# Kernel tuning notes

Hardware: AMD Instinct MI355X
Metric: run time of the kernel (lower is better)

The kernel has to match this reference:

```python
import jax, jax.numpy as jnp
import numpy as np

ADAPT_RATE = 0.05


def setup_inputs() -> dict:
    key = jax.random.key(0)
    k1, k2, k3 = jax.random.split(key, 3)
    B, T, DIN, DOUT = 64, 256, 1024, 1024
    x = jax.random.normal(k1, (B, T, DIN), dtype=jnp.float32)
    W = jax.random.normal(k2, (DOUT, DIN), dtype=jnp.float32) / np.sqrt(DIN)
    b = jax.random.normal(k3, (DOUT,), dtype=jnp.float32) * 0.01
    threshold = jnp.ones((DOUT,), dtype=jnp.float32)
    return {"x": x, "W": W, "b": b, "threshold": threshold}


def reference(x, W, b, threshold):
    # Precompute the per-timestep linear once as a single big GEMM: [B,T,O]
    pre = jnp.einsum('bti,oi->bto', x, W) + b
    B, T, O = pre.shape

    def step(carry, pre_t):
        mem, thr = carry
        mem = mem + pre_t                       # membrane accumulate [B,O]
        s = (mem >= thr).astype(pre_t.dtype)    # hard threshold spike
        # adaptive threshold: in-place .data update in torch (no grad path)
        thr = thr + ADAPT_RATE * (s.mean(axis=0) - 0.5)
        mem = mem * (1.0 - s)                   # reset where spiked
        return (mem, thr), s

    mem0 = jnp.zeros((B, O), dtype=x.dtype)
    (_, _), spikes = jax.lax.scan(step, (mem0, threshold), jnp.swapaxes(pre, 0, 1))
    return jnp.swapaxes(spikes, 0, 1)  # [B,T,O]
```

## Files before the change

### kernel.cpp

```cpp
#include <hip/hip_runtime.h>

#define B_ 64
#define T_ 256
#define DIN_ 1024
#define DOUT_ 1024

typedef int v4i  __attribute__((ext_vector_type(4)));
typedef int v16i __attribute__((ext_vector_type(16)));

#define PRE_BYTES 134217728ULL
#define XS_BYTES  83886080ULL
#define WSL_BYTES 5242880ULL
#define SPM_BYTES 2097152ULL

__device__ __forceinline__ void async_copy16(const void* g, void* l) {
    __builtin_amdgcn_global_load_lds(
        (const __attribute__((address_space(1))) void*)g,
        (__attribute__((address_space(3))) void*)l, 16, 0, 0);
}

__global__ __launch_bounds__(256) void snn_split_x(
    const float* __restrict__ x, char* __restrict__ xs)
{
    const int W    = blockIdx.x * 4 + (threadIdx.x >> 6);
    const int lane = threadIdx.x & 63;
    const int mt = W & 1, kt = (W >> 1) & 31, t0 = W >> 6;
    const int m = lane & 31, kh = lane >> 5;
    const int b = mt * 32 + m;

    const float* src = x + ((size_t)b * T_ + t0) * DIN_ + kt * 32 + kh * 16;
    float f[16];
    *(float4*)(f)      = *(const float4*)(src);
    *(float4*)(f + 4)  = *(const float4*)(src + 4);
    *(float4*)(f + 8)  = *(const float4*)(src + 8);
    *(float4*)(f + 12) = *(const float4*)(src + 12);

    unsigned pk[4][4];
#pragma unroll
    for (int s = 0; s < 4; ++s)
        pk[s][0] = pk[s][1] = pk[s][2] = pk[s][3] = 0u;
#pragma unroll
    for (int j = 0; j < 16; ++j) {
        float v = f[j] * 0.125f;
#pragma unroll
        for (int s = 0; s < 4; ++s) {
            const float ml = (s == 0) ? 64.f : 128.f;
            const float sv = __builtin_rintf(v * ml);
            v = v * ml - sv;
            const int iv = (int)sv;
            pk[s][j >> 2] |= ((unsigned)iv & 0xffu) << ((j & 3) * 8);
        }
    }
#pragma unroll
    for (int s = 0; s < 4; ++s) {
        char* dst = xs + (size_t)(((s * 256 + t0) * 32 + kt) * 2 + mt) * 1024
                       + lane * 16;
        *(uint4*)dst = make_uint4(pk[s][0], pk[s][1], pk[s][2], pk[s][3]);
    }
}

__global__ __launch_bounds__(256) void snn_split_w(
    const float* __restrict__ Wt, char* __restrict__ wsl)
{
    const int W    = blockIdx.x * 4 + (threadIdx.x >> 6);
    const int lane = threadIdx.x & 63;
    const int kt = W & 31, ot = W >> 5;
    const int n = lane & 31, kh = lane >> 5;
    const int o = ot * 32 + n;

    const float* src = Wt + (size_t)o * DIN_ + kt * 32 + kh * 16;
    float f[16];
    *(float4*)(f)      = *(const float4*)(src);
    *(float4*)(f + 4)  = *(const float4*)(src + 4);
    *(float4*)(f + 8)  = *(const float4*)(src + 8);
    *(float4*)(f + 12) = *(const float4*)(src + 12);

    unsigned pk[4][4];
#pragma unroll
    for (int s = 0; s < 4; ++s)
        pk[s][0] = pk[s][1] = pk[s][2] = pk[s][3] = 0u;
#pragma unroll
    for (int j = 0; j < 16; ++j) {
        float v = f[j] * 4.0f;
#pragma unroll
        for (int s = 0; s < 4; ++s) {
            const float ml = (s == 0) ? 64.f : 128.f;
            const float sv = __builtin_rintf(v * ml);
            v = v * ml - sv;
            const int iv = (int)sv;
            pk[s][j >> 2] |= ((unsigned)iv & 0xffu) << ((j & 3) * 8);
        }
    }
#pragma unroll
    for (int s = 0; s < 4; ++s) {
        char* dst = wsl + (size_t)((s * 32 + ot) * 32 + kt) * 1024 + lane * 16;
        *(uint4*)dst = make_uint4(pk[s][0], pk[s][1], pk[s][2], pk[s][3]);
    }
}

__global__ __launch_bounds__(256, 4) void snn_gemm_i8(
    const char* __restrict__ xs, const char* __restrict__ wsl,
    const float* __restrict__ bias, double* __restrict__ pre)
{
    __shared__ __align__(16) char ldsA[3][8 * 1024];
    __shared__ __align__(16) char ldsB[2][8 * 1024];
    const int t0 = blockIdx.x >> 4;
    const int oc = blockIdx.x & 15;
    const int tid = threadIdx.x;
    const int lane = tid & 63;
    const int ws = __builtin_amdgcn_readfirstlane(tid >> 6);
    const int wm = ws >> 1;
    const int wo = ws & 1;
    const int lo = lane * 16;

    v16i acc[4];
#pragma unroll
    for (int g = 0; g < 4; ++g)
#pragma unroll
        for (int r = 0; r < 16; ++r) acc[g][r] = 0;

    const char* sgA = xs  + (size_t)(t0 * 64 + ws) * 1024 + lo;
    const char* sgB = wsl + (size_t)((oc * 2 + (ws - 2)) * 32) * 1024 + lo;

    if (ws < 2) {
#pragma unroll
        for (int s = 0; s < 4; ++s)
            async_copy16(sgA + (size_t)s * 16777216, &ldsA[0][(ws * 4 + s) * 1024]);
#pragma unroll
        for (int s = 0; s < 4; ++s)
            async_copy16(sgA + (size_t)s * 16777216 + 2048,
                         &ldsA[1][(ws * 4 + s) * 1024]);
    } else {
#pragma unroll
        for (int s = 0; s < 4; ++s)
            async_copy16(sgB + (size_t)s * 1048576,
                         &ldsB[0][((ws - 2) * 4 + s) * 1024]);
    }

    int rdA = 0;
    int stA = 2;
    for (int kt = 0; kt < 32; ++kt) {
        if (ws < 2) {
            if (kt < 31) asm volatile("s_waitcnt vmcnt(4)" ::: "memory");
            else         asm volatile("s_waitcnt vmcnt(0)" ::: "memory");
        } else {
            asm volatile("s_waitcnt vmcnt(0)" ::: "memory");
        }
        __builtin_amdgcn_s_barrier();
        asm volatile("" ::: "memory");

        if (ws < 2) {
            if (kt + 2 < 32) {
                const size_t ko = (size_t)(kt + 2) * 2048;
#pragma unroll
                for (int s = 0; s < 4; ++s)
                    async_copy16(sgA + (size_t)s * 16777216 + ko,
                                 &ldsA[stA][(ws * 4 + s) * 1024]);
            }
        } else {
            if (kt + 1 < 32) {
                const size_t ko = (size_t)(kt + 1) * 1024;
#pragma unroll
                for (int s = 0; s < 4; ++s)
                    async_copy16(sgB + (size_t)s * 1048576 + ko,
                                 &ldsB[(kt + 1) & 1][((ws - 2) * 4 + s) * 1024]);
            }
        }

        const char* bufA = ldsA[rdA];
        const char* bufB = ldsB[kt & 1];
        v4i a[4], b[4];
#pragma unroll
        for (int s = 0; s < 4; ++s)
            a[s] = *(const v4i*)(bufA + (wm * 4 + s) * 1024 + lo);
#pragma unroll
        for (int s = 0; s < 4; ++s)
            b[s] = *(const v4i*)(bufB + (wo * 4 + s) * 1024 + lo);

        __builtin_amdgcn_s_setprio(1);
#define MF(I, J)                                                               \
        acc[(I) + (J)] = __builtin_amdgcn_mfma_i32_32x32x32_i8(                \
            a[I], b[J], acc[(I) + (J)], 0, 0, 0)
        MF(0, 3); MF(0, 2); MF(0, 1);
        MF(1, 2); MF(1, 1); MF(1, 0);
        MF(2, 1); MF(2, 0); MF(0, 0);
        MF(3, 0);
#undef MF
        __builtin_amdgcn_s_setprio(0);

        rdA = (rdA == 2) ? 0 : rdA + 1;
        stA = (stA == 2) ? 0 : stA + 1;
    }

    const int n = lane & 31, lh = lane >> 5;
    const int o = oc * 64 + wo * 32 + n;
    const double bv = (double)bias[o];
    double* dst = pre + ((size_t)t0 * DOUT_ + o) * 64 + wm * 32;
#pragma unroll
    for (int r = 0; r < 16; ++r) {
        const int row = (r & 3) + 8 * (r >> 2) + 4 * lh;
        double v = (double)acc[3][r];
        v = v * 0.0078125 + (double)acc[2][r];
        v = v * 0.0078125 + (double)acc[1][r];
        v = v * 0.0078125 + (double)acc[0][r];
        dst[row] = v * 0x1p-11 + bv;
    }
}

__global__ __launch_bounds__(256, 2) void snn_gemm_fb(
    const float* __restrict__ x, const float* __restrict__ W,
    const float* __restrict__ bias, double* __restrict__ pre)
{
    __shared__ float smem[2][8 * 72 + 8 * 256];
    const int t0 = blockIdx.x & 255;
    const int o0 = blockIdx.x >> 8;
    const int tid = threadIdx.x;
    const int to = tid & 31;
    const int tb = tid >> 5;

    double acc[8][8];
#pragma unroll
    for (int i = 0; i < 8; ++i)
#pragma unroll
        for (int j = 0; j < 8; ++j) acc[i][j] = 0.0;

    const int arow = tid >> 2;
    const int ak2  = (tid & 3) * 2;
    const float* xg = x + (size_t)(t0 + 256 * arow) * DIN_ + ak2;
    const float* wg = W + (size_t)(o0 * 256 + tid) * DIN_;

    float2 f2  = *(const float2*)(xg);
    float4 bq0 = *(const float4*)(wg);
    float4 bq1 = *(const float4*)(wg + 4);

    for (int kc = 0; kc < DIN_ / 8; ++kc) {
        float* base = smem[kc & 1];
        float (*AsF)[72]  = (float(*)[72])base;
        float (*BsF)[256] = (float(*)[256])(base + 8 * 72);
        AsF[ak2 + 0][arow] = f2.x;
        AsF[ak2 + 1][arow] = f2.y;
        BsF[0][tid] = bq0.x;  BsF[1][tid] = bq0.y;
        BsF[2][tid] = bq0.z;  BsF[3][tid] = bq0.w;
        BsF[4][tid] = bq1.x;  BsF[5][tid] = bq1.y;
        BsF[6][tid] = bq1.z;  BsF[7][tid] = bq1.w;
        __syncthreads();
        if (kc + 1 < DIN_ / 8) {
            f2  = *(const float2*)(xg + (kc + 1) * 8);
            bq0 = *(const float4*)(wg + (kc + 1) * 8);
            bq1 = *(const float4*)(wg + (kc + 1) * 8 + 4);
        }
#pragma unroll
        for (int k = 0; k < 8; ++k) {
            const float4 af0 = *(const float4*)&AsF[k][tb * 8];
            const float4 af1 = *(const float4*)&AsF[k][tb * 8 + 4];
            const float4 bf0 = *(const float4*)&BsF[k][to * 4];
            const float4 bf1 = *(const float4*)&BsF[k][128 + to * 4];
            double a[8], b[8];
            a[0] = (double)af0.x; a[1] = (double)af0.y;
            a[2] = (double)af0.z; a[3] = (double)af0.w;
            a[4] = (double)af1.x; a[5] = (double)af1.y;
            a[6] = (double)af1.z; a[7] = (double)af1.w;
            b[0] = (double)bf0.x; b[1] = (double)bf0.y;
            b[2] = (double)bf0.z; b[3] = (double)bf0.w;
            b[4] = (double)bf1.x; b[5] = (double)bf1.y;
            b[6] = (double)bf1.z; b[7] = (double)bf1.w;
#pragma unroll
            for (int i = 0; i < 8; ++i)
#pragma unroll
                for (int j = 0; j < 8; ++j)
                    acc[i][j] += a[i] * b[j];
        }
        __syncthreads();
    }

    double biasd[8];
#pragma unroll
    for (int j = 0; j < 8; ++j)
        biasd[j] = (double)bias[o0 * 256 + (j >> 2) * 128 + to * 4 + (j & 3)];
    double (*trans)[67] = (double(*)[67])smem[0];
    for (int c = 0; c < 16; ++c) {
        __syncthreads();
        const int j4  = c >> 3;
        const int tlo = (c & 7) * 4;
        if (to >= tlo && to < tlo + 4) {
#pragma unroll
            for (int p4 = 0; p4 < 4; ++p4) {
                const int r = (to - tlo) * 4 + p4;
                const int j = j4 * 4 + p4;
#pragma unroll
                for (int i = 0; i < 8; ++i)
                    trans[r][tb * 8 + i] = acc[i][j] + biasd[j];
            }
        }
        __syncthreads();
#pragma unroll
        for (int q = 0; q < 4; ++q) {
            const int idx = tid + 256 * q;
            const int b  = idx & 63;
            const int oc = idx >> 6;
            pre[(size_t)(t0 * DOUT_ + o0 * 256 + c * 16 + oc) * 64 + b] = trans[oc][b];
        }
    }
}

#define SCAN_LOAD(PV, TB)                                                      \
    do {                                                                       \
        _Pragma("unroll")                                                      \
        for (int j = 0; j < 16; ++j)                                           \
            PV[j] = p[(size_t)((TB) + j) * (DOUT_ * 64)];                      \
    } while (0)

#define SCAN_STEP(PV, TB)                                                      \
    do {                                                                       \
        _Pragma("unroll")                                                      \
        for (int j = 0; j < 16; ++j) {                                         \
            mem += PV[j];                                                      \
            const bool s = (mem >= thr);                                       \
            const unsigned long long msk = __ballot(s);                        \
            thr += 0.05 * ((double)__popcll(msk) * (1.0 / 64.0) - 0.5);        \
            if (spM) {                                                         \
                if (lane == 0) spM[(size_t)((TB) + j) * DOUT_ + o] = msk;      \
            } else {                                                           \
                outD[(size_t)lane * (T_ * DOUT_) +                             \
                     (size_t)((TB) + j) * DOUT_ + o] = s ? 1.0f : 0.0f;        \
            }                                                                  \
            mem = s ? 0.0 : mem;                                               \
        }                                                                      \
    } while (0)

__global__ __launch_bounds__(256) void snn_scan(
    const double* __restrict__ pre, const float* __restrict__ thr_in,
    unsigned long long* __restrict__ spM, float* __restrict__ outD)
{
    const int wid  = (blockIdx.x * blockDim.x + threadIdx.x) >> 6;
    const int lane = threadIdx.x & 63;
    if (wid >= DOUT_) return;
    const int o = wid;

    double mem = 0.0;
    double thr = (double)thr_in[o];
    const double* p = pre + (size_t)o * 64 + lane;

    double pvA[16], pvB[16];
    SCAN_LOAD(pvA, 0);
    for (int t = 0; t < T_; t += 32) {
        if (t + 16 < T_) SCAN_LOAD(pvB, t + 16);
        SCAN_STEP(pvA, t);
        if (t + 32 < T_) SCAN_LOAD(pvA, t + 32);
        SCAN_STEP(pvB, t + 16);
    }
}

__global__ __launch_bounds__(256) void snn_expand(
    const unsigned long long* __restrict__ spM, float* __restrict__ out)
{
    const int idx = blockIdx.x * 256 + threadIdx.x;
    const int og = idx & 255;
    const int t  = idx >> 8;
    const unsigned long long* mp = spM + (size_t)t * DOUT_ + og * 4;
    const unsigned long long m0 = mp[0], m1 = mp[1], m2 = mp[2], m3 = mp[3];
    float* op = out + (size_t)t * DOUT_ + og * 4;
#pragma unroll
    for (int b = 0; b < 64; ++b) {
        float4 v;
        v.x = (float)((m0 >> b) & 1ULL);
        v.y = (float)((m1 >> b) & 1ULL);
        v.z = (float)((m2 >> b) & 1ULL);
        v.w = (float)((m3 >> b) & 1ULL);
        *(float4*)(op + (size_t)b * (T_ * DOUT_)) = v;
    }
}

extern "C" void kernel_launch(void* const* d_in, const int* in_sizes, int n_in,
                              void* d_out, int out_size, void* d_ws, size_t ws_size,
                              hipStream_t stream) {
    const float* x    = (const float*)d_in[0];
    const float* W    = (const float*)d_in[1];
    const float* bias = (const float*)d_in[2];
    const float* thr  = (const float*)d_in[3];
    float* out = (float*)d_out;

    double* pre = (double*)d_ws;
    const size_t need = PRE_BYTES + XS_BYTES + WSL_BYTES + SPM_BYTES;

    if (ws_size >= need) {
        char* xs  = (char*)d_ws + PRE_BYTES;
        char* wsl = xs + XS_BYTES;
        unsigned long long* spM = (unsigned long long*)(wsl + WSL_BYTES);
        snn_split_x<<<4096, 256, 0, stream>>>(x, xs);
        snn_split_w<<<256, 256, 0, stream>>>(W, wsl);
        snn_gemm_i8<<<4096, 256, 0, stream>>>(xs, wsl, bias, pre);
        snn_scan<<<256, 256, 0, stream>>>(pre, thr, spM, nullptr);
        snn_expand<<<256, 256, 0, stream>>>(spM, out);
    } else {
        const bool two_stage = (ws_size >= PRE_BYTES + SPM_BYTES);
        unsigned long long* spM =
            two_stage ? (unsigned long long*)((char*)d_ws + PRE_BYTES) : nullptr;
        snn_gemm_fb<<<1024, 256, 0, stream>>>(x, W, bias, pre);
        snn_scan<<<256, 256, 0, stream>>>(pre, thr, spM, two_stage ? nullptr : out);
        if (two_stage)
            snn_expand<<<1024, 256, 0, stream>>>(spM, out);
    }
}
```

Before: 340.0 us.

## Replace LDS-staged async pipeline in int8 GEMM with direct register double-buffering

The int8 split-precision GEMM kernel no longer stages A and B tiles through LDS with global_load_lds, waitcnt and per-iteration barriers. Each wave now loads its own fragments straight from global memory into two register sets and alternates between them, overlapping the next tile's loads with the current MFMAs. This removes the barriers and LDS traffic but duplicates global loads across waves that share tiles (A is read by both wo waves, B by both wm waves) and raises register pressure, so launch bounds drop from 4 to 3 blocks per SIMD.

Result: slower. 372.7 us (+9.6%).

```diff
diff --git a/kernel.cpp b/kernel.cpp
--- a/kernel.cpp
+++ b/kernel.cpp
@@ -12,12 +12,6 @@
 #define XS_BYTES  83886080ULL
 #define WSL_BYTES 5242880ULL
 #define SPM_BYTES 2097152ULL
-
-__device__ __forceinline__ void async_copy16(const void* g, void* l) {
-    __builtin_amdgcn_global_load_lds(
-        (const __attribute__((address_space(1))) void*)g,
-        (__attribute__((address_space(3))) void*)l, 16, 0, 0);
-}
 
 __global__ __launch_bounds__(256) void snn_split_x(
     const float* __restrict__ x, char* __restrict__ xs)
@@ -98,12 +92,10 @@
     }
 }
 
-__global__ __launch_bounds__(256, 4) void snn_gemm_i8(
+__global__ __launch_bounds__(256, 3) void snn_gemm_i8(
     const char* __restrict__ xs, const char* __restrict__ wsl,
     const float* __restrict__ bias, double* __restrict__ pre)
 {
-    __shared__ __align__(16) char ldsA[3][8 * 1024];
-    __shared__ __align__(16) char ldsB[2][8 * 1024];
     const int t0 = blockIdx.x >> 4;
     const int oc = blockIdx.x & 15;
     const int tid = threadIdx.x;
@@ -119,78 +111,54 @@
 #pragma unroll
         for (int r = 0; r < 16; ++r) acc[g][r] = 0;
 
-    const char* sgA = xs  + (size_t)(t0 * 64 + ws) * 1024 + lo;
-    const char* sgB = wsl + (size_t)((oc * 2 + (ws - 2)) * 32) * 1024 + lo;
-
-    if (ws < 2) {
-#pragma unroll
-        for (int s = 0; s < 4; ++s)
-            async_copy16(sgA + (size_t)s * 16777216, &ldsA[0][(ws * 4 + s) * 1024]);
-#pragma unroll
-        for (int s = 0; s < 4; ++s)
-            async_copy16(sgA + (size_t)s * 16777216 + 2048,
-                         &ldsA[1][(ws * 4 + s) * 1024]);
-    } else {
-#pragma unroll
-        for (int s = 0; s < 4; ++s)
-            async_copy16(sgB + (size_t)s * 1048576,
-                         &ldsB[0][((ws - 2) * 4 + s) * 1024]);
-    }
-
-    int rdA = 0;
-    int stA = 2;
-    for (int kt = 0; kt < 32; ++kt) {
-        if (ws < 2) {
-            if (kt < 31) asm volatile("s_waitcnt vmcnt(4)" ::: "memory");
-            else         asm volatile("s_waitcnt vmcnt(0)" ::: "memory");
-        } else {
-            asm volatile("s_waitcnt vmcnt(0)" ::: "memory");
-        }
-        __builtin_amdgcn_s_barrier();
-        asm volatile("" ::: "memory");
-
-        if (ws < 2) {
-            if (kt + 2 < 32) {
-                const size_t ko = (size_t)(kt + 2) * 2048;
-#pragma unroll
-                for (int s = 0; s < 4; ++s)
-                    async_copy16(sgA + (size_t)s * 16777216 + ko,
-                                 &ldsA[stA][(ws * 4 + s) * 1024]);
-            }
-        } else {
-            if (kt + 1 < 32) {
-                const size_t ko = (size_t)(kt + 1) * 1024;
-#pragma unroll
-                for (int s = 0; s < 4; ++s)
-                    async_copy16(sgB + (size_t)s * 1048576 + ko,
-                                 &ldsB[(kt + 1) & 1][((ws - 2) * 4 + s) * 1024]);
-            }
-        }
-
-        const char* bufA = ldsA[rdA];
-        const char* bufB = ldsB[kt & 1];
-        v4i a[4], b[4];
-#pragma unroll
-        for (int s = 0; s < 4; ++s)
-            a[s] = *(const v4i*)(bufA + (wm * 4 + s) * 1024 + lo);
-#pragma unroll
-        for (int s = 0; s < 4; ++s)
-            b[s] = *(const v4i*)(bufB + (wo * 4 + s) * 1024 + lo);
-
-        __builtin_amdgcn_s_setprio(1);
-#define MF(I, J)                                                               \
-        acc[(I) + (J)] = __builtin_amdgcn_mfma_i32_32x32x32_i8(                \
-            a[I], b[J], acc[(I) + (J)], 0, 0, 0)
-        MF(0, 3); MF(0, 2); MF(0, 1);
-        MF(1, 2); MF(1, 1); MF(1, 0);
-        MF(2, 1); MF(2, 0); MF(0, 0);
-        MF(3, 0);
-#undef MF
-        __builtin_amdgcn_s_setprio(0);
-
-        rdA = (rdA == 2) ? 0 : rdA + 1;
-        stA = (stA == 2) ? 0 : stA + 1;
-    }
+    const char* ab = xs  + (size_t)(t0 * 64 + wm) * 1024 + lo;
+    const char* bb = wsl + (size_t)((oc * 2 + wo) * 32) * 1024 + lo;
+
+    v4i aP[4], bP[4], aQ[4], bQ[4];
+
+#define LOAD_A(R, KT)                                                          \
+    do { _Pragma("unroll")                                                     \
+        for (int s = 0; s < 4; ++s)                                            \
+            R[s] = *(const v4i*)(ab + (size_t)s * 16777216 +                   \
+                                 (size_t)(KT) * 2048);                         \
+    } while (0)
+#define LOAD_B(R, KT)                                                          \
+    do { _Pragma("unroll")                                                     \
+        for (int s = 0; s < 4; ++s)                                            \
+            R[s] = *(const v4i*)(bb + (size_t)s * 1048576 +                    \
+                                 (size_t)(KT) * 1024);                         \
+    } while (0)
+#define MFMA10(A, B)                                                           \
+    do {                                                                       \
+        __builtin_amdgcn_s_setprio(1);                                         \
+        acc[3] = __builtin_amdgcn_mfma_i32_32x32x32_i8(A[0], B[3], acc[3],0,0,0);\
+        acc[2] = __builtin_amdgcn_mfma_i32_32x32x32_i8(A[0], B[2], acc[2],0,0,0);\
+        acc[1] = __builtin_amdgcn_mfma_i32_32x32x32_i8(A[0], B[1], acc[1],0,0,0);\
+        acc[3] = __builtin_amdgcn_mfma_i32_32x32x32_i8(A[1], B[2], acc[3],0,0,0);\
+        acc[2] = __builtin_amdgcn_mfma_i32_32x32x32_i8(A[1], B[1], acc[2],0,0,0);\
+        acc[1] = __builtin_amdgcn_mfma_i32_32x32x32_i8(A[1], B[0], acc[1],0,0,0);\
+        acc[3] = __builtin_amdgcn_mfma_i32_32x32x32_i8(A[2], B[1], acc[3],0,0,0);\
+        acc[2] = __builtin_amdgcn_mfma_i32_32x32x32_i8(A[2], B[0], acc[2],0,0,0);\
+        acc[0] = __builtin_amdgcn_mfma_i32_32x32x32_i8(A[0], B[0], acc[0],0,0,0);\
+        acc[3] = __builtin_amdgcn_mfma_i32_32x32x32_i8(A[3], B[0], acc[3],0,0,0);\
+        __builtin_amdgcn_s_setprio(0);                                         \
+    } while (0)
+
+    LOAD_A(aP, 0); LOAD_B(bP, 0);
+    for (int ks = 0; ks < 15; ++ks) {
+        const int kt = 2 * ks;
+        LOAD_A(aQ, kt + 1); LOAD_B(bQ, kt + 1);
+        MFMA10(aP, bP);
+        LOAD_A(aP, kt + 2); LOAD_B(bP, kt + 2);
+        MFMA10(aQ, bQ);
+    }
+    LOAD_A(aQ, 31); LOAD_B(bQ, 31);
+    MFMA10(aP, bP);
+    MFMA10(aQ, bQ);
+
+#undef LOAD_A
+#undef LOAD_B
+#undef MFMA10
 
     const int n = lane & 31, lh = lane >> 5;
     const int o = oc * 64 + wo * 32 + n;
```

## Widen i8 GEMM tile to 64x128 with 8 waves and triple-buffered B

Applied to the files above, without the earlier changes.

The int8 split-precision GEMM block goes from 4 to 8 waves and covers 128 output columns instead of 64, which halves the grid. Each A tile staged in LDS is now reused across twice as many output columns, cutting global A traffic. B moves from double to triple buffering so A and B share one 2-ahead prefetch schedule, with waits adjusted per wave role. The costs are more LDS per block (72KB), which may limit occupancy, and fewer blocks to spread across CUs.

After: 340.2 us. About the same (+0.1%).

```diff
diff --git a/kernel.cpp b/kernel.cpp
--- a/kernel.cpp
+++ b/kernel.cpp
@@ -98,19 +98,19 @@
     }
 }
 
-__global__ __launch_bounds__(256, 4) void snn_gemm_i8(
+__global__ __launch_bounds__(512, 4) void snn_gemm_i8(
     const char* __restrict__ xs, const char* __restrict__ wsl,
     const float* __restrict__ bias, double* __restrict__ pre)
 {
     __shared__ __align__(16) char ldsA[3][8 * 1024];
-    __shared__ __align__(16) char ldsB[2][8 * 1024];
-    const int t0 = blockIdx.x >> 4;
-    const int oc = blockIdx.x & 15;
+    __shared__ __align__(16) char ldsB[3][16 * 1024];
+    const int t0 = blockIdx.x >> 3;
+    const int oc = blockIdx.x & 7;
     const int tid = threadIdx.x;
     const int lane = tid & 63;
     const int ws = __builtin_amdgcn_readfirstlane(tid >> 6);
-    const int wm = ws >> 1;
-    const int wo = ws & 1;
+    const int wm = ws >> 2;
+    const int wo = ws & 3;
     const int lo = lane * 16;
 
     v16i acc[4];
@@ -119,56 +119,47 @@
 #pragma unroll
         for (int r = 0; r < 16; ++r) acc[g][r] = 0;
 
-    const char* sgA = xs  + (size_t)(t0 * 64 + ws) * 1024 + lo;
-    const char* sgB = wsl + (size_t)((oc * 2 + (ws - 2)) * 32) * 1024 + lo;
-
-    if (ws < 2) {
-#pragma unroll
-        for (int s = 0; s < 4; ++s)
-            async_copy16(sgA + (size_t)s * 16777216, &ldsA[0][(ws * 4 + s) * 1024]);
-#pragma unroll
-        for (int s = 0; s < 4; ++s)
-            async_copy16(sgA + (size_t)s * 16777216 + 2048,
-                         &ldsA[1][(ws * 4 + s) * 1024]);
-    } else {
-#pragma unroll
-        for (int s = 0; s < 4; ++s)
-            async_copy16(sgB + (size_t)s * 1048576,
-                         &ldsB[0][((ws - 2) * 4 + s) * 1024]);
-    }
-
-    int rdA = 0;
-    int stA = 2;
+    const int mtA = ws >> 1;
+    const int sA  = (ws & 1) * 2;
+    const char* sgA0 = xs + (size_t)(sA + 0) * 16777216
+                          + (size_t)t0 * 65536 + (size_t)mtA * 1024 + lo;
+    const char* sgA1 = xs + (size_t)(sA + 1) * 16777216
+                          + (size_t)t0 * 65536 + (size_t)mtA * 1024 + lo;
+    const char* sgB = wsl + (size_t)(oc * 4 + (ws - 4)) * 32768 + lo;
+
+#define STAGE_BATCH(JB, BUF)                                                   \
+    do {                                                                       \
+        if (ws < 4) {                                                          \
+            async_copy16(sgA0 + (size_t)(JB) * 2048,                           \
+                         &ldsA[BUF][(mtA * 4 + sA + 0) * 1024]);               \
+            async_copy16(sgA1 + (size_t)(JB) * 2048,                           \
+                         &ldsA[BUF][(mtA * 4 + sA + 1) * 1024]);               \
+        } else {                                                               \
+            _Pragma("unroll")                                                  \
+            for (int s = 0; s < 4; ++s)                                        \
+                async_copy16(sgB + (size_t)s * 1048576 + (size_t)(JB) * 1024,  \
+                             &ldsB[BUF][((ws - 4) * 4 + s) * 1024]);           \
+        }                                                                      \
+    } while (0)
+
+    STAGE_BATCH(0, 0);
+    STAGE_BATCH(1, 1);
+
+    int rd = 0, st = 2;
     for (int kt = 0; kt < 32; ++kt) {
-        if (ws < 2) {
-            if (kt < 31) asm volatile("s_waitcnt vmcnt(4)" ::: "memory");
-            else         asm volatile("s_waitcnt vmcnt(0)" ::: "memory");
+        if (kt < 31) {
+            if (ws < 4) asm volatile("s_waitcnt vmcnt(2)" ::: "memory");
+            else        asm volatile("s_waitcnt vmcnt(4)" ::: "memory");
         } else {
             asm volatile("s_waitcnt vmcnt(0)" ::: "memory");
         }
         __builtin_amdgcn_s_barrier();
         asm volatile("" ::: "memory");
 
-        if (ws < 2) {
-            if (kt + 2 < 32) {
-                const size_t ko = (size_t)(kt + 2) * 2048;
-#pragma unroll
-                for (int s = 0; s < 4; ++s)
-                    async_copy16(sgA + (size_t)s * 16777216 + ko,
-                                 &ldsA[stA][(ws * 4 + s) * 1024]);
-            }
-        } else {
-            if (kt + 1 < 32) {
-                const size_t ko = (size_t)(kt + 1) * 1024;
-#pragma unroll
-                for (int s = 0; s < 4; ++s)
-                    async_copy16(sgB + (size_t)s * 1048576 + ko,
-                                 &ldsB[(kt + 1) & 1][((ws - 2) * 4 + s) * 1024]);
-            }
-        }
-
-        const char* bufA = ldsA[rdA];
-        const char* bufB = ldsB[kt & 1];
+        if (kt + 2 < 32) STAGE_BATCH(kt + 2, st);
+
+        const char* bufA = ldsA[rd];
+        const char* bufB = ldsB[rd];
         v4i a[4], b[4];
 #pragma unroll
         for (int s = 0; s < 4; ++s)
@@ -188,12 +179,13 @@
 #undef MF
         __builtin_amdgcn_s_setprio(0);
 
-        rdA = (rdA == 2) ? 0 : rdA + 1;
-        stA = (stA == 2) ? 0 : stA + 1;
-    }
+        rd = (rd == 2) ? 0 : rd + 1;
+        st = (st == 2) ? 0 : st + 1;
+    }
+#undef STAGE_BATCH
 
     const int n = lane & 31, lh = lane >> 5;
-    const int o = oc * 64 + wo * 32 + n;
+    const int o = oc * 128 + wo * 32 + n;
     const double bv = (double)bias[o];
     double* dst = pre + ((size_t)t0 * DOUT_ + o) * 64 + wm * 32;
 #pragma unroll
@@ -389,7 +381,7 @@
         unsigned long long* spM = (unsigned long long*)(wsl + WSL_BYTES);
         snn_split_x<<<4096, 256, 0, stream>>>(x, xs);
         snn_split_w<<<256, 256, 0, stream>>>(W, wsl);
-        snn_gemm_i8<<<4096, 256, 0, stream>>>(xs, wsl, bias, pre);
+        snn_gemm_i8<<<2048, 512, 0, stream>>>(xs, wsl, bias, pre);
         snn_scan<<<256, 256, 0, stream>>>(pre, thr, spM, nullptr);
         snn_expand<<<256, 256, 0, stream>>>(spM, out);
     } else {
```
